# Kernel optimization log

Hardware: AMD Instinct MI355X
Metric: run time of the kernel (lower is better)

## Reference

```python
import jax, jax.numpy as jnp
import numpy as np
from functools import lru_cache
from jax.scipy.linalg import expm

N_QUBITS = 6
DIM = 2 ** N_QUBITS          # 64
N_PAULI = 4 ** N_QUBITS      # 4096


@lru_cache(maxsize=None)
def _pauli_tensor_np(n_qubits):
    # All n-qubit Pauli strings as dense matrices, ordered base-4
    # (digit 0..3 -> I, X, Y, Z; most-significant digit = first qubit).
    I = np.eye(2, dtype=np.complex64)
    X = np.array([[0, 1], [1, 0]], dtype=np.complex64)
    Y = np.array([[0, -1j], [1j, 0]], dtype=np.complex64)
    Z = np.array([[1, 0], [0, -1]], dtype=np.complex64)
    base = np.stack([I, X, Y, Z])  # [4,2,2]
    T = base
    for _ in range(n_qubits - 1):
        k, d = T.shape[0], T.shape[1]
        T = np.einsum('iab,jcd->ijacbd', T, base).reshape(k * 4, d * 2, d * 2)
    return np.ascontiguousarray(T.astype(np.complex64))  # [4^n, 2^n, 2^n]


def setup_inputs() -> dict:
    key = jax.random.key(0)
    kx, kw, kb = jax.random.split(key, 3)
    x = jax.random.normal(kx, (512, 4000), dtype=jnp.float32)
    weight = jax.random.normal(kw, (4, N_PAULI - 1), dtype=jnp.float32)
    bias = jax.random.normal(kb, (DIM,), dtype=jnp.float32)
    return {"x": x, "weight": weight, "bias": bias}


def reference(x, weight, bias):
    # x: [B, in_dim] float32; weight: [n_reps, 4^n - 1]; bias: [out_dim]
    B, in_dim = x.shape
    n_reps = weight.shape[0]
    out_dim = bias.shape[0]
    P = jnp.asarray(_pauli_tensor_np(N_QUBITS))  # [4096, 64, 64] complex64

    # Pad data coefficients up to the full Pauli basis (identity included).
    xp = jnp.pad(x, ((0, 0), (0, N_PAULI - in_dim))).astype(jnp.complex64)

    # Data-encoding Hamiltonian per sample: H_d[b] = sum_p x[b,p] * P[p]
    Hd = jnp.einsum('bp,pij->bij', xp, P)                       # [B,64,64]
    Ud = jax.vmap(expm)(-1j * Hd)                               # [B,64,64]

    # Trainable Hamiltonians per rep (identity Pauli excluded -> global phase).
    Hp = jnp.einsum('rp,pij->rij', weight.astype(jnp.complex64), P[1:])
    Up = jax.vmap(expm)(-1j * Hp)                               # [R,64,64]

    # Data re-uploading circuit on |0...0>: repeat (U_param @ U_data).
    psi = jnp.zeros((B, DIM), dtype=jnp.complex64).at[:, 0].set(1.0)
    for r in range(n_reps):
        psi = jnp.einsum('bij,bj->bi', Ud, psi)
        psi = jnp.einsum('ij,bj->bi', Up[r], psi)

    # Observables are computational-basis projectors |k><k|, k < out_dim:
    # <psi|O_k|psi> = |psi_k|^2
    probs = (psi[:, :out_dim].real ** 2 + psi[:, :out_dim].imag ** 2)
    return probs.astype(jnp.float32) + bias
```

## Files before the change

kernel.cpp:

```cpp
#include <hip/hip_runtime.h>
#include <math.h>

typedef float2 cplx;
typedef __attribute__((ext_vector_type(8))) short short8v;
typedef __attribute__((ext_vector_type(4))) short short4v;
typedef __attribute__((ext_vector_type(4))) float float4v;

#define TPB 256
#define IN_DIM 4000
#define NREPS 4

#define C0f  1.0f
#define C1f  1.0f
#define C2f  0.5f
#define C3f  0.16666667f
#define C4f  0.041666668f
#define C5f  8.3333333e-3f
#define C6f  1.3888889e-3f
#define C7f  1.9841270e-4f
#define C8f  2.4801587e-5f
#define C9f  2.7557319e-6f
#define C10f 2.7557319e-7f
#define C11f 2.5052108e-8f
#define C12f 2.0876757e-9f
#define C13f 1.6059044e-10f
#define C14f 1.1470746e-11f
#define C15f 7.6471637e-13f

#define MFMA(A,B,C) __builtin_amdgcn_mfma_f32_16x16x32_bf16((A),(B),(C),0,0,0)


__device__ __forceinline__ int idxSw(int a, int b) {
    return (a << 6) + ((((b >> 3) + a) & 7) << 3) + (b & 7);
}
__device__ __forceinline__ short f2bf(float f) {
    unsigned u = __float_as_uint(f);
    return (short)((u + 0x7FFF + ((u >> 16) & 1)) >> 16);
}
__device__ __forceinline__ float bf2f(short s) {
    return __uint_as_float(((unsigned)(unsigned short)s) << 16);
}
__device__ __forceinline__ short8v neg8(short8v a) {
    int4 u; __builtin_memcpy(&u, &a, 16);
    u.x ^= 0x80008000; u.y ^= 0x80008000; u.z ^= 0x80008000; u.w ^= 0x80008000;
    short8v r; __builtin_memcpy(&r, &u, 16); return r;
}

template<int MODE>
__device__ __forceinline__ void mm_mfma(const short* __restrict__ As,
                                        const short* __restrict__ Bs,
                                        int li, int q, int mh, int nh,
                                        float4v* __restrict__ accR,
                                        float4v* __restrict__ accI)
{
    #pragma unroll
    for (int ks = 0; ks < 2; ks++) {
        const int ch = ks * 4 + q;
        short8v arh[2], arl[2], aih[2], ail[2], nih[2], nil_[2];
        #pragma unroll
        for (int dm = 0; dm < 2; dm++) {
            int r = ((mh * 2 + dm) << 4) + li;
            int off = (r << 6) + (((ch + r) & 7) << 3);
            arh[dm] = *(const short8v*)(As + off);
            arl[dm] = *(const short8v*)(As + 4096 + off);
            aih[dm] = *(const short8v*)(As + 8192 + off);
            ail[dm] = *(const short8v*)(As + 12288 + off);
            nih[dm] = neg8(aih[dm]);
            nil_[dm] = neg8(ail[dm]);
        }
        #pragma unroll
        for (int dn = 0; dn < 2; dn++) {
            int n = ((nh * 2 + dn) << 4) + li;
            int off = (n << 6) + (((ch + n) & 7) << 3);
            short8v brh = *(const short8v*)(Bs + off);
            short8v brl = *(const short8v*)(Bs + 4096 + off);
            short8v bih = *(const short8v*)(Bs + 8192 + off);
            short8v bil = *(const short8v*)(Bs + 12288 + off);
            if (MODE == 1) { brh = neg8(brh); brl = neg8(brl); }
            if (MODE == 2) { bih = neg8(bih); bil = neg8(bil); }
            #pragma unroll
            for (int dm = 0; dm < 2; dm++) {
                int ti = dm * 2 + dn;
                accR[ti] = MFMA(arh[dm], brh, accR[ti]);
                accR[ti] = MFMA(arh[dm], brl, accR[ti]);
                accR[ti] = MFMA(arl[dm], brh, accR[ti]);
                accR[ti] = MFMA(nih[dm], bih, accR[ti]);
                accR[ti] = MFMA(nih[dm], bil, accR[ti]);
                accR[ti] = MFMA(nil_[dm], bih, accR[ti]);
                accI[ti] = MFMA(arh[dm], bih, accI[ti]);
                accI[ti] = MFMA(arh[dm], bil, accI[ti]);
                accI[ti] = MFMA(arl[dm], bih, accI[ti]);
                accI[ti] = MFMA(aih[dm], brh, accI[ti]);
                accI[ti] = MFMA(aih[dm], brl, accI[ti]);
                accI[ti] = MFMA(ail[dm], brh, accI[ti]);
            }
        }
    }
}

__device__ __forceinline__ void write_row(short* __restrict__ S, int li, int q,
                                          int mh, int nh,
                                          const float4v* cre, const float4v* cim)
{
    #pragma unroll
    for (int dm = 0; dm < 2; dm++)
    #pragma unroll
    for (int dn = 0; dn < 2; dn++) {
        int ti = dm * 2 + dn;
        int c = ((nh * 2 + dn) << 4) + li;
        #pragma unroll
        for (int reg = 0; reg < 4; reg++) {
            int r = ((mh * 2 + dm) << 4) + q * 4 + reg;
            int off = idxSw(r, c);
            float vr = cre[ti][reg], vi = cim[ti][reg];
            short rh = f2bf(vr), rl = f2bf(vr - bf2f(rh));
            short ih = f2bf(vi), il = f2bf(vi - bf2f(ih));
            S[off] = rh; S[4096 + off] = rl; S[8192 + off] = ih; S[12288 + off] = il;
        }
    }
}

__device__ __forceinline__ void write_rowT(short* __restrict__ S, int li, int q,
                                           int mh, int nh,
                                           const float4v* cre, const float4v* cim)
{
    #pragma unroll
    for (int dm = 0; dm < 2; dm++)
    #pragma unroll
    for (int dn = 0; dn < 2; dn++) {
        int ti = dm * 2 + dn;
        int c = ((nh * 2 + dn) << 4) + li;
        int k0 = ((mh * 2 + dm) << 4) + q * 4;
        int off = idxSw(c, k0);
        short4v rh, rl, ih, il;
        #pragma unroll
        for (int reg = 0; reg < 4; reg++) {
            float vr = cre[ti][reg], vi = cim[ti][reg];
            short h1 = f2bf(vr); rh[reg] = h1; rl[reg] = f2bf(vr - bf2f(h1));
            short h2 = f2bf(vi); ih[reg] = h2; il[reg] = f2bf(vi - bf2f(h2));
        }
        *(short4v*)(S + off) = rh;
        *(short4v*)(S + 4096 + off) = rl;
        *(short4v*)(S + 8192 + off) = ih;
        *(short4v*)(S + 12288 + off) = il;
    }
}

__device__ __forceinline__ void gather_tile(const short* __restrict__ S, int li, int q,
                                            int mh, int nh, float4v* bre, float4v* bim)
{
    #pragma unroll
    for (int dm = 0; dm < 2; dm++)
    #pragma unroll
    for (int dn = 0; dn < 2; dn++) {
        int ti = dm * 2 + dn;
        int c = ((nh * 2 + dn) << 4) + li;
        #pragma unroll
        for (int reg = 0; reg < 4; reg++) {
            int r = ((mh * 2 + dm) << 4) + q * 4 + reg;
            int off = idxSw(r, c);
            bre[ti][reg] = bf2f(S[off]) + bf2f(S[4096 + off]);
            bim[ti][reg] = bf2f(S[8192 + off]) + bf2f(S[12288 + off]);
        }
    }
}

__device__ __forceinline__ void adddiag(float4v* ure, float cI, int li, int q, int mh, int nh)
{
    #pragma unroll
    for (int dm = 0; dm < 2; dm++)
    #pragma unroll
    for (int dn = 0; dn < 2; dn++) {
        if (2 * mh + dm == 2 * nh + dn) {
            #pragma unroll
            for (int e = 0; e < 4; e++)
                if (li == q * 4 + e) ure[dm * 2 + dn][e] += cI;
        }
    }
}

__device__ __forceinline__ void pauli_masks(int p, int& xm, int& zm) {
    xm = 0; zm = 0;
    #pragma unroll
    for (int k = 0; k < 6; k++) {
        int lo = (p >> (2 * k)) & 1;
        int hi = (p >> (2 * k + 1)) & 1;
        zm |= hi << k;
        xm |= (hi ^ lo) << k;
    }
}
__device__ __forceinline__ cplx pauli_phase(float v, int xm, int zm) {
    int ny = __popc(xm & zm) & 3;
    if (ny == 0) return make_float2(v, 0.f);
    if (ny == 1) return make_float2(0.f, -v);
    if (ny == 2) return make_float2(-v, 0.f);
    return make_float2(0.f, v);
}

__global__ __launch_bounds__(TPB) void expm_mfma_kernel(const float* __restrict__ x,
                                                        const float* __restrict__ w,
                                                        cplx* __restrict__ ws, int B)
{
    __shared__ float4 LDSf4[4098];
    char* LDS = (char*)LDSf4;
    short* S0 = (short*)LDS;
    short* S1 = S0 + 16384;
    cplx* W = (cplx*)(LDS + 32768);
    float* red = (float*)(LDS + 65536);
    const int t = threadIdx.x, blk = blockIdx.x;
    const int lane = t & 63, wv = t >> 6;

    float sumsq = 0.f;
    {
        const bool isW = (blk >= B);
        const float* src = isW ? (w + (size_t)(blk - B) * 4095)
                               : (x + (size_t)blk * IN_DIM);
        #pragma unroll
        for (int n = 0; n < 16; n++) {
            int p = t + TPB * n;
            float v = isW ? ((p == 0) ? 0.f : src[p - 1])
                          : ((p < IN_DIM) ? src[p] : 0.f);
            sumsq += v * v;
            int xm, zm; pauli_masks(p, xm, zm);
            W[(xm << 6) + zm] = pauli_phase(v, xm, zm);
        }
        #pragma unroll
        for (int d = 32; d >= 1; d >>= 1) sumsq += __shfl_xor(sumsq, d, 64);
        if (lane == 0) red[wv] = sumsq;
    }
    __syncthreads();

    float fro = sqrtf(64.f * (red[0] + red[1] + red[2] + red[3]));
    int s1 = 0; { float nn = fro; while (nn > 8.f && s1 < 24) { nn *= 0.5f; s1++; } }
    float sc1 = exp2f((float)(-s1));

    cplx hv[16];
    #pragma unroll
    for (int rr = 0; rr < 16; rr++) hv[rr] = W[(((wv << 4) + rr) << 6) + lane];
    #pragma unroll
    for (int d = 1; d < 64; d <<= 1) {
        float sg = (lane & d) ? -1.f : 1.f;
        #pragma unroll
        for (int rr = 0; rr < 16; rr++) {
            float px = __shfl_xor(hv[rr].x, d, 64);
            float py = __shfl_xor(hv[rr].y, d, 64);
            hv[rr].x = fmaf(sg, hv[rr].x, px);
            hv[rr].y = fmaf(sg, hv[rr].y, py);
        }
    }
    __syncthreads();

    #pragma unroll
    for (int rr = 0; rr < 16; rr++) {
        int m = (wv << 4) + rr;
        int c = lane ^ m;
        float vr = hv[rr].y * sc1, vi = -hv[rr].x * sc1;
        short rh = f2bf(vr), rl = f2bf(vr - bf2f(rh));
        short ih = f2bf(vi), il = f2bf(vi - bf2f(ih));
        int off = idxSw(lane, c);
        S0[off] = rh; S0[4096 + off] = rl; S0[8192 + off] = ih; S0[12288 + off] = il;
    }
    __syncthreads();

    const int li = lane & 15, q = lane >> 4;
    const int mh = wv & 1, nh = wv >> 1;
    const float4v z4 = {0.f, 0.f, 0.f, 0.f};
    float4v accR[4], accI[4];
    #define ZERO_ACC _Pragma("unroll") for (int i2 = 0; i2 < 4; i2++) { accR[i2]=z4; accI[i2]=z4; }

    ZERO_ACC
    mm_mfma<1>(S0, S0, li, q, mh, nh, accR, accI);
    float ss = 0.f;
    #pragma unroll
    for (int ti = 0; ti < 4; ti++)
        #pragma unroll
        for (int e = 0; e < 4; e++)
            ss += accR[ti][e]*accR[ti][e] + accI[ti][e]*accI[ti][e];
    #pragma unroll
    for (int d = 32; d >= 1; d >>= 1) ss += __shfl_xor(ss, d, 64);
    if (lane == 0) red[4 + wv] = ss;
    __syncthreads();

    float bound = sqrtf(sqrtf(red[4] + red[5] + red[6] + red[7]));
    int ds = 0; { float nn = bound; while (nn > 3.4f && ds < 12) { nn *= 0.5f; ds++; } }
    const int s = s1 + ds;
    float dsc = exp2f((float)(-ds)), dsc2 = dsc * dsc;

    float4v bre[4], bim[4];
    gather_tile(S0, li, q, mh, nh, bre, bim);
    __syncthreads();

    float4v ure[4], uim[4];
    #pragma unroll
    for (int ti = 0; ti < 4; ti++) { ure[ti] = accR[ti] * dsc2; uim[ti] = accI[ti] * dsc2; }
    write_row(S1, li, q, mh, nh, ure, uim);
    {
        float ca = C15f * dsc;
        #pragma unroll
        for (int ti = 0; ti < 4; ti++) { ure[ti] = ca * bre[ti]; uim[ti] = ca * bim[ti]; }
        adddiag(ure, C14f, li, q, mh, nh);
        write_row(S0, li, q, mh, nh, ure, uim);
    }
    __syncthreads();

    const float cIc[7] = { C0f, C2f, C4f, C6f, C8f, C10f, C12f };
    const float cAc[7] = { C1f, C3f, C5f, C7f, C9f, C11f, C13f };
    for (int j = 6; j >= 0; j--) {
        ZERO_ACC
        mm_mfma<2>(S0, S1, li, q, mh, nh, accR, accI);
        __syncthreads();
        float ca = cAc[j] * dsc, cI = cIc[j];
        #pragma unroll
        for (int ti = 0; ti < 4; ti++) {
            ure[ti] = accR[ti] + ca * bre[ti];
            uim[ti] = accI[ti] + ca * bim[ti];
        }
        adddiag(ure, cI, li, q, mh, nh);
        write_row(S0, li, q, mh, nh, ure, uim);
        __syncthreads();
    }

    write_rowT(S1, li, q, mh, nh, ure, uim);
    __syncthreads();
    for (int sq = 0; sq < s; sq++) {
        ZERO_ACC
        mm_mfma<0>(S0, S1, li, q, mh, nh, accR, accI);
        __syncthreads();
        #pragma unroll
        for (int ti = 0; ti < 4; ti++) { ure[ti] = accR[ti]; uim[ti] = accI[ti]; }
        if (sq < s - 1) {
            write_row(S0, li, q, mh, nh, ure, uim);
            write_rowT(S1, li, q, mh, nh, ure, uim);
            __syncthreads();
        }
    }
    #undef ZERO_ACC

    cplx* dst = ws + ((size_t)blk << 12);
    #pragma unroll
    for (int dm = 0; dm < 2; dm++)
    #pragma unroll
    for (int dn = 0; dn < 2; dn++) {
        int ti = dm * 2 + dn;
        int c = ((nh * 2 + dn) << 4) + li;
        int cs = c ^ (((c >> 4) & 1) << 1);
        #pragma unroll
        for (int reg = 0; reg < 4; reg++) {
            int r = ((mh * 2 + dm) << 4) + q * 4 + reg;
            dst[(r << 6) + cs] = make_float2(ure[ti][reg], uim[ti][reg]);
        }
    }
}

__device__ __forceinline__ cplx matvec_partial(const cplx* __restrict__ M,
                                               const cplx* __restrict__ pin,
                                               int i, int g)
{
    float ax = 0.f, ay = 0.f;
    const float4* Mr = (const float4*)(M + (i << 6));
    #pragma unroll
    for (int c = 0; c < 4; c++) {
        int ch = ((g << 2) + c + (i & 15)) & 15;
        int b = (ch >> 2) & 1;
        float4 m01 = Mr[(ch << 1) + b];
        float4 m23 = Mr[(ch << 1) + 1 - b];
        const cplx* p = pin + (ch << 2);
        cplx p0 = p[0], p1 = p[1], p2 = p[2], p3 = p[3];
        ax = fmaf(m01.x, p0.x, fmaf(-m01.y, p0.y, ax));
        ay = fmaf(m01.x, p0.y, fmaf( m01.y, p0.x, ay));
        ax = fmaf(m01.z, p1.x, fmaf(-m01.w, p1.y, ax));
        ay = fmaf(m01.z, p1.y, fmaf( m01.w, p1.x, ay));
        ax = fmaf(m23.x, p2.x, fmaf(-m23.y, p2.y, ax));
        ay = fmaf(m23.x, p2.y, fmaf( m23.y, p2.x, ay));
        ax = fmaf(m23.z, p3.x, fmaf(-m23.w, p3.y, ax));
        ay = fmaf(m23.z, p3.y, fmaf( m23.w, p3.x, ay));
    }
    return make_float2(ax, ay);
}

__global__ __launch_bounds__(TPB) void matvec_kernel(const cplx* __restrict__ ws,
                                                     const float* __restrict__ bias,
                                                     float* __restrict__ out, int B)
{
    __shared__ float4 Xs4[2048];
    __shared__ float4 Ys4[2048];
    __shared__ cplx psiA[64], psiB[64];
    __shared__ cplx part[256];
    cplx* X = (cplx*)Xs4;
    cplx* Y = (cplx*)Ys4;
    const int t = threadIdx.x, b = blockIdx.x;
    const int i = t & 63, g = t >> 6;
    {
        const float4* src = (const float4*)(ws + ((size_t)b << 12));
        float4* dst = (float4*)X;
        #pragma unroll
        for (int n = 0; n < 8; n++) dst[n * TPB + t] = src[n * TPB + t];
    }
    if (t < 64) psiA[t] = make_float2(t == 0 ? 1.f : 0.f, 0.f);
    __syncthreads();

    for (int r = 0; r < NREPS; r++) {
        {
            const float4* src = (const float4*)(ws + ((size_t)(B + r) << 12));
            float4* dstY = (float4*)Y;
            #pragma unroll
            for (int n = 0; n < 8; n++) dstY[n * TPB + t] = src[n * TPB + t];
        }
        part[t] = matvec_partial(X, psiA, i, g);
        __syncthreads();
        if (t < 64) {
            cplx a0 = part[t], a1 = part[64 + t], a2 = part[128 + t], a3 = part[192 + t];
            psiB[t] = make_float2(a0.x + a1.x + a2.x + a3.x, a0.y + a1.y + a2.y + a3.y);
        }
        __syncthreads();
        part[t] = matvec_partial(Y, psiB, i, g);
        __syncthreads();
        if (t < 64) {
            cplx a0 = part[t], a1 = part[64 + t], a2 = part[128 + t], a3 = part[192 + t];
            psiA[t] = make_float2(a0.x + a1.x + a2.x + a3.x, a0.y + a1.y + a2.y + a3.y);
        }
        __syncthreads();
    }
    if (t < 64) {
        cplx pv = psiA[t];
        out[(b << 6) + t] = fmaf(pv.x, pv.x, fmaf(pv.y, pv.y, bias[t]));
    }
}

extern "C" void kernel_launch(void* const* d_in, const int* in_sizes, int n_in,
                              void* d_out, int out_size, void* d_ws, size_t ws_size,
                              hipStream_t stream)
{
    const float* x    = (const float*)d_in[0];
    const float* w    = (const float*)d_in[1];
    const float* bias = (const float*)d_in[2];
    float* out = (float*)d_out;
    cplx* ws   = (cplx*)d_ws;

    int B = in_sizes[0] / IN_DIM;

    hipLaunchKernelGGL(expm_mfma_kernel, dim3(B + NREPS), dim3(TPB), 0, stream, x, w, ws, B);
    hipLaunchKernelGGL(matvec_kernel,    dim3(B),         dim3(TPB), 0, stream, ws, bias, out, B);
}
```

Measured before the change: 161.1 us.

## Fuse per-sample expm with circuit matvec and split out parameter-unitary kernel

The data-unitary exponential is now computed and consumed inside one circuit kernel, so the 512 per-sample 64x64 unitaries no longer go through global memory between two launches. The four parameter unitaries get their own small kernel that runs first. The MFMA helper now takes separate conjugation/negation modes for A and B, and the LDS buffer roles and transposed writes are rearranged so the squaring loop reads its operands in a different layout. The fused kernel uses more LDS per block, and the tiny up_kernel launch is serialised ahead of the main work.

```diff
diff --git a/kernel.cpp b/kernel.cpp
--- a/kernel.cpp
+++ b/kernel.cpp
@@ -46,7 +46,7 @@
     short8v r; __builtin_memcpy(&r, &u, 16); return r;
 }
 
-template<int MODE>
+template<int AM, int BM>
 __device__ __forceinline__ void mm_mfma(const short* __restrict__ As,
                                         const short* __restrict__ Bs,
                                         int li, int q, int mh, int nh,
@@ -56,17 +56,20 @@
     #pragma unroll
     for (int ks = 0; ks < 2; ks++) {
         const int ch = ks * 4 + q;
-        short8v arh[2], arl[2], aih[2], ail[2], nih[2], nil_[2];
+        short8v arh[2], arl[2], cRh[2], cRl[2], cIh[2], cIl[2];
         #pragma unroll
         for (int dm = 0; dm < 2; dm++) {
             int r = ((mh * 2 + dm) << 4) + li;
             int off = (r << 6) + (((ch + r) & 7) << 3);
             arh[dm] = *(const short8v*)(As + off);
             arl[dm] = *(const short8v*)(As + 4096 + off);
-            aih[dm] = *(const short8v*)(As + 8192 + off);
-            ail[dm] = *(const short8v*)(As + 12288 + off);
-            nih[dm] = neg8(aih[dm]);
-            nil_[dm] = neg8(ail[dm]);
+            short8v aih = *(const short8v*)(As + 8192 + off);
+            short8v ail = *(const short8v*)(As + 12288 + off);
+            short8v nih = neg8(aih), nil_ = neg8(ail);
+            cRh[dm] = (AM == 2) ? aih : nih;
+            cRl[dm] = (AM == 2) ? ail : nil_;
+            cIh[dm] = (AM == 2) ? nih : aih;
+            cIl[dm] = (AM == 2) ? nil_ : ail;
         }
         #pragma unroll
         for (int dn = 0; dn < 2; dn++) {
@@ -76,23 +79,22 @@
             short8v brl = *(const short8v*)(Bs + 4096 + off);
             short8v bih = *(const short8v*)(Bs + 8192 + off);
             short8v bil = *(const short8v*)(Bs + 12288 + off);
-            if (MODE == 1) { brh = neg8(brh); brl = neg8(brl); }
-            if (MODE == 2) { bih = neg8(bih); bil = neg8(bil); }
+            if (BM == 1) { brh = neg8(brh); brl = neg8(brl); }
             #pragma unroll
             for (int dm = 0; dm < 2; dm++) {
                 int ti = dm * 2 + dn;
                 accR[ti] = MFMA(arh[dm], brh, accR[ti]);
                 accR[ti] = MFMA(arh[dm], brl, accR[ti]);
                 accR[ti] = MFMA(arl[dm], brh, accR[ti]);
-                accR[ti] = MFMA(nih[dm], bih, accR[ti]);
-                accR[ti] = MFMA(nih[dm], bil, accR[ti]);
-                accR[ti] = MFMA(nil_[dm], bih, accR[ti]);
+                accR[ti] = MFMA(cRh[dm], bih, accR[ti]);
+                accR[ti] = MFMA(cRh[dm], bil, accR[ti]);
+                accR[ti] = MFMA(cRl[dm], bih, accR[ti]);
                 accI[ti] = MFMA(arh[dm], bih, accI[ti]);
                 accI[ti] = MFMA(arh[dm], bil, accI[ti]);
                 accI[ti] = MFMA(arl[dm], bih, accI[ti]);
-                accI[ti] = MFMA(aih[dm], brh, accI[ti]);
-                accI[ti] = MFMA(aih[dm], brl, accI[ti]);
-                accI[ti] = MFMA(ail[dm], brh, accI[ti]);
+                accI[ti] = MFMA(cIh[dm], brh, accI[ti]);
+                accI[ti] = MFMA(cIh[dm], brl, accI[ti]);
+                accI[ti] = MFMA(cIl[dm], brh, accI[ti]);
             }
         }
     }
@@ -197,37 +199,29 @@
     return make_float2(0.f, v);
 }
 
-__global__ __launch_bounds__(TPB) void expm_mfma_kernel(const float* __restrict__ x,
-                                                        const float* __restrict__ w,
-                                                        cplx* __restrict__ ws, int B)
-{
-    __shared__ float4 LDSf4[4098];
-    char* LDS = (char*)LDSf4;
+__device__ __forceinline__ void expm_core(char* __restrict__ LDS,
+                                          const float* __restrict__ src, bool isW,
+                                          int t, float4v* ure, float4v* uim)
+{
     short* S0 = (short*)LDS;
-    short* S1 = S0 + 16384;
-    cplx* W = (cplx*)(LDS + 32768);
+    short* S1 = (short*)(LDS + 32768);
+    cplx*  W  = (cplx*)(LDS + 32768);
     float* red = (float*)(LDS + 65536);
-    const int t = threadIdx.x, blk = blockIdx.x;
     const int lane = t & 63, wv = t >> 6;
 
     float sumsq = 0.f;
-    {
-        const bool isW = (blk >= B);
-        const float* src = isW ? (w + (size_t)(blk - B) * 4095)
-                               : (x + (size_t)blk * IN_DIM);
-        #pragma unroll
-        for (int n = 0; n < 16; n++) {
-            int p = t + TPB * n;
-            float v = isW ? ((p == 0) ? 0.f : src[p - 1])
-                          : ((p < IN_DIM) ? src[p] : 0.f);
-            sumsq += v * v;
-            int xm, zm; pauli_masks(p, xm, zm);
-            W[(xm << 6) + zm] = pauli_phase(v, xm, zm);
-        }
-        #pragma unroll
-        for (int d = 32; d >= 1; d >>= 1) sumsq += __shfl_xor(sumsq, d, 64);
-        if (lane == 0) red[wv] = sumsq;
-    }
+    #pragma unroll
+    for (int n = 0; n < 16; n++) {
+        int p = t + TPB * n;
+        float v = isW ? ((p == 0) ? 0.f : src[p - 1])
+                      : ((p < IN_DIM) ? src[p] : 0.f);
+        sumsq += v * v;
+        int xm, zm; pauli_masks(p, xm, zm);
+        W[(xm << 6) + zm] = pauli_phase(v, xm, zm);
+    }
+    #pragma unroll
+    for (int d = 32; d >= 1; d >>= 1) sumsq += __shfl_xor(sumsq, d, 64);
+    if (lane == 0) red[wv] = sumsq;
     __syncthreads();
 
     float fro = sqrtf(64.f * (red[0] + red[1] + red[2] + red[3]));
@@ -269,7 +263,7 @@
     #define ZERO_ACC _Pragma("unroll") for (int i2 = 0; i2 < 4; i2++) { accR[i2]=z4; accI[i2]=z4; }
 
     ZERO_ACC
-    mm_mfma<1>(S0, S0, li, q, mh, nh, accR, accI);
+    mm_mfma<0, 1>(S0, S0, li, q, mh, nh, accR, accI);
     float ss = 0.f;
     #pragma unroll
     for (int ti = 0; ti < 4; ti++)
@@ -288,18 +282,18 @@
 
     float4v bre[4], bim[4];
     gather_tile(S0, li, q, mh, nh, bre, bim);
-    __syncthreads();
-
-    float4v ure[4], uim[4];
+
     #pragma unroll
     for (int ti = 0; ti < 4; ti++) { ure[ti] = accR[ti] * dsc2; uim[ti] = accI[ti] * dsc2; }
-    write_row(S1, li, q, mh, nh, ure, uim);
+    write_rowT(S1, li, q, mh, nh, ure, uim);
+    __syncthreads();
+
     {
         float ca = C15f * dsc;
         #pragma unroll
         for (int ti = 0; ti < 4; ti++) { ure[ti] = ca * bre[ti]; uim[ti] = ca * bim[ti]; }
         adddiag(ure, C14f, li, q, mh, nh);
-        write_row(S0, li, q, mh, nh, ure, uim);
+        write_rowT(S0, li, q, mh, nh, ure, uim);
     }
     __syncthreads();
 
@@ -307,7 +301,7 @@
     const float cAc[7] = { C1f, C3f, C5f, C7f, C9f, C11f, C13f };
     for (int j = 6; j >= 0; j--) {
         ZERO_ACC
-        mm_mfma<2>(S0, S1, li, q, mh, nh, accR, accI);
+        mm_mfma<2, 0>(S1, S0, li, q, mh, nh, accR, accI);
         __syncthreads();
         float ca = cAc[j] * dsc, cI = cIc[j];
         #pragma unroll
@@ -316,40 +310,21 @@
             uim[ti] = accI[ti] + ca * bim[ti];
         }
         adddiag(ure, cI, li, q, mh, nh);
-        write_row(S0, li, q, mh, nh, ure, uim);
-        __syncthreads();
-    }
-
-    write_rowT(S1, li, q, mh, nh, ure, uim);
-    __syncthreads();
+        write_rowT(S0, li, q, mh, nh, ure, uim);
+        __syncthreads();
+    }
+
     for (int sq = 0; sq < s; sq++) {
+        write_row(S1, li, q, mh, nh, ure, uim);
+        if (sq > 0) write_rowT(S0, li, q, mh, nh, ure, uim);
+        __syncthreads();
         ZERO_ACC
-        mm_mfma<0>(S0, S1, li, q, mh, nh, accR, accI);
+        mm_mfma<0, 0>(S1, S0, li, q, mh, nh, accR, accI);
         __syncthreads();
         #pragma unroll
         for (int ti = 0; ti < 4; ti++) { ure[ti] = accR[ti]; uim[ti] = accI[ti]; }
-        if (sq < s - 1) {
-            write_row(S0, li, q, mh, nh, ure, uim);
-            write_rowT(S1, li, q, mh, nh, ure, uim);
-            __syncthreads();
-        }
     }
     #undef ZERO_ACC
-
-    cplx* dst = ws + ((size_t)blk << 12);
-    #pragma unroll
-    for (int dm = 0; dm < 2; dm++)
-    #pragma unroll
-    for (int dn = 0; dn < 2; dn++) {
-        int ti = dm * 2 + dn;
-        int c = ((nh * 2 + dn) << 4) + li;
-        int cs = c ^ (((c >> 4) & 1) << 1);
-        #pragma unroll
-        for (int reg = 0; reg < 4; reg++) {
-            int r = ((mh * 2 + dm) << 4) + q * 4 + reg;
-            dst[(r << 6) + cs] = make_float2(ure[ti][reg], uim[ti][reg]);
-        }
-    }
 }
 
 __device__ __forceinline__ cplx matvec_partial(const cplx* __restrict__ M,
@@ -378,42 +353,83 @@
     return make_float2(ax, ay);
 }
 
-__global__ __launch_bounds__(TPB) void matvec_kernel(const cplx* __restrict__ ws,
-                                                     const float* __restrict__ bias,
-                                                     float* __restrict__ out, int B)
-{
-    __shared__ float4 Xs4[2048];
-    __shared__ float4 Ys4[2048];
-    __shared__ cplx psiA[64], psiB[64];
-    __shared__ cplx part[256];
-    cplx* X = (cplx*)Xs4;
-    cplx* Y = (cplx*)Ys4;
+__global__ __launch_bounds__(TPB) void up_kernel(const float* __restrict__ w,
+                                                 cplx* __restrict__ ws)
+{
+    __shared__ float4 LDSf4[4290];
+    char* LDS = (char*)LDSf4;
+    const int t = threadIdx.x, r = blockIdx.x;
+    float4v ure[4], uim[4];
+    expm_core(LDS, w + (size_t)r * 4095, true, t, ure, uim);
+
+    const int lane = t & 63, wv = t >> 6, li = lane & 15, q = lane >> 4;
+    const int mh = wv & 1, nh = wv >> 1;
+    cplx* dst = ws + ((size_t)r << 12);
+    #pragma unroll
+    for (int dm = 0; dm < 2; dm++)
+    #pragma unroll
+    for (int dn = 0; dn < 2; dn++) {
+        int ti = dm * 2 + dn;
+        int c = ((nh * 2 + dn) << 4) + li;
+        int cs = c ^ (((c >> 4) & 1) << 1);
+        #pragma unroll
+        for (int reg = 0; reg < 4; reg++) {
+            int rr = ((mh * 2 + dm) << 4) + q * 4 + reg;
+            dst[(rr << 6) + cs] = make_float2(ure[ti][reg], uim[ti][reg]);
+        }
+    }
+}
+
+__global__ __launch_bounds__(TPB) void circuit_kernel(const float* __restrict__ x,
+                                                      const cplx* __restrict__ ws,
+                                                      const float* __restrict__ bias,
+                                                      float* __restrict__ out)
+{
+    __shared__ float4 LDSf4[4290];
+    char* LDS = (char*)LDSf4;
     const int t = threadIdx.x, b = blockIdx.x;
+    float4v ure[4], uim[4];
+    expm_core(LDS, x + (size_t)b * IN_DIM, false, t, ure, uim);
+
+    cplx* Ud   = (cplx*)(LDS + 32768);
+    cplx* UpS  = (cplx*)LDS;
+    cplx* psiA = (cplx*)(LDS + 65568);
+    cplx* psiB = (cplx*)(LDS + 66080);
+    cplx* part = (cplx*)(LDS + 66592);
+
+    const int lane = t & 63, wv = t >> 6, li = lane & 15, q = lane >> 4;
+    const int mh = wv & 1, nh = wv >> 1;
+    #pragma unroll
+    for (int dm = 0; dm < 2; dm++)
+    #pragma unroll
+    for (int dn = 0; dn < 2; dn++) {
+        int ti = dm * 2 + dn;
+        int c = ((nh * 2 + dn) << 4) + li;
+        int cs = c ^ (((c >> 4) & 1) << 1);
+        #pragma unroll
+        for (int reg = 0; reg < 4; reg++) {
+            int rr = ((mh * 2 + dm) << 4) + q * 4 + reg;
+            Ud[(rr << 6) + cs] = make_float2(ure[ti][reg], uim[ti][reg]);
+        }
+    }
+    if (t < 64) psiA[t] = make_float2(t == 0 ? 1.f : 0.f, 0.f);
+    __syncthreads();
+
     const int i = t & 63, g = t >> 6;
-    {
-        const float4* src = (const float4*)(ws + ((size_t)b << 12));
-        float4* dst = (float4*)X;
-        #pragma unroll
-        for (int n = 0; n < 8; n++) dst[n * TPB + t] = src[n * TPB + t];
-    }
-    if (t < 64) psiA[t] = make_float2(t == 0 ? 1.f : 0.f, 0.f);
-    __syncthreads();
-
     for (int r = 0; r < NREPS; r++) {
-        {
-            const float4* src = (const float4*)(ws + ((size_t)(B + r) << 12));
-            float4* dstY = (float4*)Y;
-            #pragma unroll
-            for (int n = 0; n < 8; n++) dstY[n * TPB + t] = src[n * TPB + t];
-        }
-        part[t] = matvec_partial(X, psiA, i, g);
+        const float4* srcv = (const float4*)(ws + ((size_t)r << 12));
+        float4* dstY = (float4*)UpS;
+        #pragma unroll
+        for (int n = 0; n < 8; n++) dstY[n * TPB + t] = srcv[n * TPB + t];
+        __syncthreads();
+        part[t] = matvec_partial(Ud, psiA, i, g);
         __syncthreads();
         if (t < 64) {
             cplx a0 = part[t], a1 = part[64 + t], a2 = part[128 + t], a3 = part[192 + t];
             psiB[t] = make_float2(a0.x + a1.x + a2.x + a3.x, a0.y + a1.y + a2.y + a3.y);
         }
         __syncthreads();
-        part[t] = matvec_partial(Y, psiB, i, g);
+        part[t] = matvec_partial(UpS, psiB, i, g);
         __syncthreads();
         if (t < 64) {
             cplx a0 = part[t], a1 = part[64 + t], a2 = part[128 + t], a3 = part[192 + t];
@@ -439,6 +455,6 @@
 
     int B = in_sizes[0] / IN_DIM;
 
-    hipLaunchKernelGGL(expm_mfma_kernel, dim3(B + NREPS), dim3(TPB), 0, stream, x, w, ws, B);
-    hipLaunchKernelGGL(matvec_kernel,    dim3(B),         dim3(TPB), 0, stream, ws, bias, out, B);
-}
+    hipLaunchKernelGGL(up_kernel,      dim3(NREPS), dim3(TPB), 0, stream, w, ws);
+    hipLaunchKernelGGL(circuit_kernel, dim3(B),     dim3(TPB), 0, stream, x, ws, bias, out);
+}
```

New measurement: 166.1 us. 1.03x slower.
